# Kernel optimization log

Measured on AMD Instinct MI355X. Metric: run time of the kernel, lower is better.

Reference implementation:

```python
import jax, jax.numpy as jnp
import numpy as np

N_NODES = 50000


def gcn_conv(x, W, b, src, dst):
    # PyG GCNConv: lin (no bias) -> add self-loops -> symmetric deg norm ->
    # scatter-add messages to target nodes -> add bias.
    n = x.shape[0]
    xw = x @ W  # [N, H]
    loops = jnp.arange(n, dtype=src.dtype)
    s = jnp.concatenate([src, loops])
    d = jnp.concatenate([dst, loops])
    deg = jax.ops.segment_sum(jnp.ones(d.shape[0], dtype=x.dtype), d, num_segments=n)
    dinv = deg ** -0.5  # deg >= 1 due to self-loops
    norm = dinv[s] * dinv[d]  # [E+N]
    msg = xw[s] * norm[:, None]  # gather + scale, [E+N, H]
    out = jax.ops.segment_sum(msg, d, num_segments=n)  # scatter-add
    return out + b


def setup_inputs() -> dict:
    key = jax.random.key(0)
    ks = jax.random.split(key, 8)
    in_feats, hidden, out_feats, p = 64, 64, 32, 4
    x = jax.random.normal(ks[0], (N_NODES, in_feats), dtype=jnp.float32)
    edge_index = jax.random.randint(ks[1], (2, 800000), 0, N_NODES, dtype=jnp.int64)
    s1 = (1.0 / in_feats) ** 0.5
    s2 = (1.0 / hidden) ** 0.5
    W1 = jax.random.uniform(ks[2], (in_feats, hidden), jnp.float32, -s1, s1)
    b1 = jnp.zeros((hidden,), jnp.float32)
    W2 = jax.random.uniform(ks[3], (hidden, hidden), jnp.float32, -s2, s2)
    b2 = jnp.zeros((hidden,), jnp.float32)
    Wr = jax.random.uniform(ks[4], (hidden, out_feats * p), jnp.float32, -s2, s2)
    br = jax.random.uniform(ks[5], (out_feats * p,), jnp.float32, -s2, s2)
    return {"x": x, "edge_index": edge_index, "W1": W1, "b1": b1,
            "W2": W2, "b2": b2, "Wr": Wr, "br": br}


def reference(x, edge_index, W1, b1, W2, b2, Wr, br):
    src, dst = edge_index[0], edge_index[1]
    h = jax.nn.relu(gcn_conv(x, W1, b1, src, dst))
    h = jax.nn.relu(gcn_conv(h, W2, b2, src, dst))
    g = jnp.mean(h, axis=0, keepdims=True)  # [1, hidden]
    out = (g @ Wr + br).reshape(32, 4)  # (out_feats, p)
    return out
```

## Files before the change

### kernel.cpp

```cpp
#include <hip/hip_runtime.h>
#include <math.h>


#define CH 16384
#define MAXNB 1024

__global__ __launch_bounds__(256) void k_bucket_hist(const int* __restrict__ dst,
                                                     int* __restrict__ histmat,
                                                     int E, int NB) {
    __shared__ int ih[MAXNB];
    int t = threadIdx.x;
    for (int k = t; k < NB; k += 256) ih[k] = 0;
    __syncthreads();
    int base = blockIdx.x * CH;
    for (int i = 0; i < CH; i += 256) {
        int e = base + i + t;
        if (e < E) atomicAdd(&ih[dst[e] >> 6], 1);
    }
    __syncthreads();
    for (int k = t; k < NB; k += 256) histmat[(size_t)blockIdx.x * NB + k] = ih[k];
}

__global__ __launch_bounds__(256) void k_colscan(int* __restrict__ histmat,
                                                 int* __restrict__ tot,
                                                 int NB, int nch) {
    int k = blockIdx.x * 256 + threadIdx.x;
    if (k >= NB) return;
    int run = 0;
    for (int b = 0; b < nch; b++) {
        int v = histmat[(size_t)b * NB + k];
        histmat[(size_t)b * NB + k] = run;
        run += v;
    }
    tot[k] = run;
}

__global__ __launch_bounds__(256) void k_scanb(const int* __restrict__ tot,
                                               int* __restrict__ bstart,
                                               int* __restrict__ offsets,
                                               int NB, int E, int n) {
    __shared__ int sc[256];
    __shared__ int carry;
    int t = threadIdx.x;
    if (t == 0) carry = 0;
    __syncthreads();
    int nchunk = (NB + 255) / 256;
    for (int c = 0; c < nchunk; c++) {
        int idx = c * 256 + t;
        int v = (idx < NB) ? tot[idx] : 0;
        sc[t] = v;
        __syncthreads();
        for (int off = 1; off < 256; off <<= 1) {
            int x = (t >= off) ? sc[t - off] : 0;
            __syncthreads();
            sc[t] += x;
            __syncthreads();
        }
        if (idx < NB) bstart[idx] = sc[t] - v + carry;
        __syncthreads();
        if (t == 0) carry += sc[255];
        __syncthreads();
    }
    if (t == 0) { bstart[NB] = E; offsets[n] = E; }
}

__global__ __launch_bounds__(256) void k_bucket_scatter(const int* __restrict__ src,
                                                        const int* __restrict__ dst,
                                                        const int* __restrict__ histmat,
                                                        const int* __restrict__ bstart,
                                                        int* __restrict__ staged,
                                                        int E, int NB) {
    __shared__ int cur[MAXNB];
    int t = threadIdx.x;
    for (int k = t; k < NB; k += 256)
        cur[k] = bstart[k] + histmat[(size_t)blockIdx.x * NB + k];
    __syncthreads();
    int base = blockIdx.x * CH;
    for (int i = 0; i < CH; i += 256) {
        int e = base + i + t;
        if (e < E) {
            int d = dst[e];
            int pos = atomicAdd(&cur[d >> 6], 1);
            staged[pos] = (src[e] << 6) | (d & 63);
        }
    }
}

__global__ __launch_bounds__(256) void k_local_sort(const int* __restrict__ staged,
                                                    const int* __restrict__ bstart,
                                                    int* __restrict__ csr_src,
                                                    int* __restrict__ offsets,
                                                    float* __restrict__ dinv, int n) {
    __shared__ int cnt[64];
    __shared__ int pos[64];
    __shared__ int cur[64];
    int t = threadIdx.x;
    if (t < 64) cnt[t] = 0;
    __syncthreads();
    int k = blockIdx.x;
    int beg = bstart[k], end = bstart[k + 1];
    for (int e = beg + t; e < end; e += 256) atomicAdd(&cnt[staged[e] & 63], 1);
    __syncthreads();
    if (t == 0) {
        int run = 0;
        for (int i = 0; i < 64; i++) { pos[i] = run; run += cnt[i]; }
    }
    __syncthreads();
    if (t < 64) {
        cur[t] = pos[t];
        int node = k * 64 + t;
        if (node < n) {
            offsets[node] = beg + pos[t];
            dinv[node] = 1.0f / sqrtf((float)(cnt[t] + 1));
        }
    }
    __syncthreads();
    for (int e = beg + t; e < end; e += 256) {
        int pk = staged[e];
        int p = atomicAdd(&cur[pk & 63], 1);
        csr_src[beg + p] = pk >> 6;
    }
}

__global__ __launch_bounds__(256) void k_gemm_scale(const float* __restrict__ X,
                                                    const float* __restrict__ W,
                                                    const float* __restrict__ dinv,
                                                    float* __restrict__ Y, int n) {
    __shared__ float Ws[64 * 64];
    __shared__ float xs[16][64];
    int t = threadIdx.x, w = t >> 6, f = t & 63;
    const float4* W4 = (const float4*)W;
    float4* Ws4 = (float4*)Ws;
#pragma unroll
    for (int j = 0; j < 4; j++) Ws4[t + 256 * j] = W4[t + 256 * j];
    int r0 = blockIdx.x * 16;
#pragma unroll
    for (int i = 0; i < 4; i++) {
        int r = r0 + w * 4 + i;
        xs[w * 4 + i][f] = (r < n) ? X[(size_t)r * 64 + f] : 0.f;
    }
    __syncthreads();
    float acc[4] = {0.f, 0.f, 0.f, 0.f};
#pragma unroll 8
    for (int k = 0; k < 64; k++) {
        float wv = Ws[k * 64 + f];
#pragma unroll
        for (int i = 0; i < 4; i++) acc[i] += xs[w * 4 + i][k] * wv;
    }
#pragma unroll
    for (int i = 0; i < 4; i++) {
        int r = r0 + w * 4 + i;
        if (r < n) Y[(size_t)r * 64 + f] = dinv[r] * acc[i];
    }
}

template <bool POOL>
__global__ __launch_bounds__(256) void k_aggregate(const float* __restrict__ Y,
                                                   const float* __restrict__ dinv,
                                                   const float* __restrict__ bias,
                                                   const int* __restrict__ offsets,
                                                   const int* __restrict__ csr_src,
                                                   float* __restrict__ H,
                                                   float* __restrict__ pbuf, int n) {
    __shared__ float sm[256];
    int t = threadIdx.x, w = t >> 6, f = t & 63;
    int node = blockIdx.x * 4 + w;
    bool valid = node < n;
    float hval = 0.f;
    if (valid) {
        int beg = offsets[node], end = offsets[node + 1];
        float acc = Y[(size_t)node * 64 + f];
        for (int j = beg; j < end; j += 8) {
#pragma unroll
            for (int u = 0; u < 8; u++) {
                int jj = j + u;
                bool c = jj < end;
                int jc = c ? jj : beg;
                int s = csr_src[jc];
                float a = Y[(size_t)s * 64 + f];
                acc += c ? a : 0.f;
            }
        }
        hval = fmaxf(dinv[node] * acc + bias[f], 0.f);
        if (!POOL) H[(size_t)node * 64 + f] = hval;
    }
    if (POOL) {
        sm[t] = valid ? hval : 0.f;
        __syncthreads();
        if (w == 0) pbuf[(size_t)blockIdx.x * 64 + f] =
            sm[f] + sm[64 + f] + sm[128 + f] + sm[192 + f];
    }
}

__global__ void k_mean_final(const float* __restrict__ pbuf, float* __restrict__ g,
                             int nrows) {
    __shared__ float part[256];
    int t = threadIdx.x, w = t >> 6, f = t & 63;
    float local = 0.f;
    for (int r = blockIdx.x * 4 + w; r < nrows; r += gridDim.x * 4)
        local += pbuf[(size_t)r * 64 + f];
    part[t] = local;
    __syncthreads();
    if (w == 0) {
        float tot = part[f] + part[64 + f] + part[128 + f] + part[192 + f];
        atomicAdd(&g[f], tot);
    }
}

__global__ void k_readout(const float* __restrict__ g, const float* __restrict__ Wr,
                          const float* __restrict__ br, float* __restrict__ out,
                          float invn) {
    __shared__ float gl[64];
    int t = threadIdx.x;
    if (t < 64) gl[t] = g[t] * invn;
    __syncthreads();
    float acc = br[t];
#pragma unroll
    for (int k = 0; k < 64; k++) acc += gl[k] * Wr[k * 128 + t];
    out[t] = acc;
}

extern "C" void kernel_launch(void* const* d_in, const int* in_sizes, int n_in,
                              void* d_out, int out_size, void* d_ws, size_t ws_size,
                              hipStream_t stream) {
    const float* x  = (const float*)d_in[0];
    const int*   ei = (const int*)d_in[1];
    const float* W1 = (const float*)d_in[2];
    const float* b1 = (const float*)d_in[3];
    const float* W2 = (const float*)d_in[4];
    const float* b2 = (const float*)d_in[5];
    const float* Wr = (const float*)d_in[6];
    const float* br = (const float*)d_in[7];
    float* out = (float*)d_out;

    int n = in_sizes[0] / 64;
    int E = in_sizes[1] / 2;
    const int* src = ei;
    const int* dst = ei + E;

    int NB  = (n + 63) / 64;
    int nch = (E + CH - 1) / CH;

    char* p = (char*)d_ws;
    float* y = (float*)p;      p += (size_t)n * 64 * sizeof(float);
    float* h = (float*)p;      p += (size_t)n * 64 * sizeof(float);
    float* dinv = (float*)p;   p += (size_t)n * sizeof(float);
    float* g = (float*)p;      p += 64 * sizeof(float);
    int* staged = (int*)p;     p += (size_t)E * sizeof(int);
    int* csr_src = (int*)p;    p += (size_t)E * sizeof(int);
    int* offsets = (int*)p;    p += (size_t)(n + 1) * sizeof(int);
    int* histmat = (int*)p;    p += (size_t)nch * NB * sizeof(int);
    int* tot = (int*)p;        p += (size_t)NB * sizeof(int);
    int* bstart = (int*)p;     p += (size_t)(NB + 1) * sizeof(int);

    int gb = (n + 3) / 4;

    hipMemsetAsync(g, 0, 64 * sizeof(float), stream);
    k_bucket_hist<<<nch, 256, 0, stream>>>(dst, histmat, E, NB);
    k_colscan<<<(NB + 255) / 256, 256, 0, stream>>>(histmat, tot, NB, nch);
    k_scanb<<<1, 256, 0, stream>>>(tot, bstart, offsets, NB, E, n);
    k_bucket_scatter<<<nch, 256, 0, stream>>>(src, dst, histmat, bstart, staged, E, NB);
    k_local_sort<<<NB, 256, 0, stream>>>(staged, bstart, csr_src, offsets, dinv, n);

    k_gemm_scale<<<(n + 15) / 16, 256, 0, stream>>>(x, W1, dinv, y, n);
    k_aggregate<false><<<gb, 256, 0, stream>>>(y, dinv, b1, offsets, csr_src, h, nullptr, n);
    k_gemm_scale<<<(n + 15) / 16, 256, 0, stream>>>(h, W2, dinv, y, n);
    float* pbuf = h;
    k_aggregate<true><<<gb, 256, 0, stream>>>(y, dinv, b2, offsets, csr_src, nullptr, pbuf, n);

    k_mean_final<<<64, 256, 0, stream>>>(pbuf, g, gb);
    k_readout<<<1, 128, 0, stream>>>(g, Wr, br, out, 1.0f / (float)n);
}
```

Before: 269.1 us.

## Vectorize aggregation with float4 edge-parallel lanes and shrink histogram chunks

The aggregation kernel now assigns 16 lanes per node row with float4 loads, and splits each node's edge list across four lane groups, combining them with cross-lane shuffles. Each wavefront therefore keeps more independent gathers in flight, and each neighbour index is loaded once per group instead of once per feature lane. The histogram chunk size is reduced to raise block count, and the column scan is unrolled by 8 so its loads batch ahead of the stores. In exchange, the column scan has more chunks to walk and more partial histograms to write.

```diff
diff --git a/kernel.cpp b/kernel.cpp
--- a/kernel.cpp
+++ b/kernel.cpp
@@ -2,7 +2,7 @@
 #include <math.h>
 
 
-#define CH 16384
+#define CH 4096
 #define MAXNB 1024
 
 __global__ __launch_bounds__(256) void k_bucket_hist(const int* __restrict__ dst,
@@ -27,10 +27,22 @@
     int k = blockIdx.x * 256 + threadIdx.x;
     if (k >= NB) return;
     int run = 0;
-    for (int b = 0; b < nch; b++) {
-        int v = histmat[(size_t)b * NB + k];
+    int b = 0;
+    for (; b + 8 <= nch; b += 8) {
+        int v[8];
+#pragma unroll
+        for (int u = 0; u < 8; u++) v[u] = histmat[(size_t)(b + u) * NB + k];
+#pragma unroll
+        for (int u = 0; u < 8; u++) {
+            int x = v[u];
+            histmat[(size_t)(b + u) * NB + k] = run;
+            run += x;
+        }
+    }
+    for (; b < nch; b++) {
+        int x = histmat[(size_t)b * NB + k];
         histmat[(size_t)b * NB + k] = run;
-        run += v;
+        run += x;
     }
     tot[k] = run;
 }
@@ -162,33 +174,57 @@
                                                    const int* __restrict__ csr_src,
                                                    float* __restrict__ H,
                                                    float* __restrict__ pbuf, int n) {
-    __shared__ float sm[256];
-    int t = threadIdx.x, w = t >> 6, f = t & 63;
+    __shared__ float4 sm4[4][16];
+    const float4* Y4 = (const float4*)Y;
+    int t = threadIdx.x, w = t >> 6, l = t & 63;
+    int q = l >> 4, c = l & 15;
     int node = blockIdx.x * 4 + w;
     bool valid = node < n;
-    float hval = 0.f;
+    float4 hval = make_float4(0.f, 0.f, 0.f, 0.f);
     if (valid) {
+        float4 acc = make_float4(0.f, 0.f, 0.f, 0.f);
+        if (q == 0) acc = Y4[(size_t)node * 16 + c];
         int beg = offsets[node], end = offsets[node + 1];
-        float acc = Y[(size_t)node * 64 + f];
-        for (int j = beg; j < end; j += 8) {
-#pragma unroll
-            for (int u = 0; u < 8; u++) {
-                int jj = j + u;
-                bool c = jj < end;
-                int jc = c ? jj : beg;
-                int s = csr_src[jc];
-                float a = Y[(size_t)s * 64 + f];
-                acc += c ? a : 0.f;
+        for (int j = beg + q; j < end; j += 16) {
+#pragma unroll
+            for (int u = 0; u < 4; u++) {
+                int jj = j + 4 * u;
+                bool ok = jj < end;
+                float4 v = make_float4(0.f, 0.f, 0.f, 0.f);
+                if (ok) {
+                    int s = csr_src[jj];
+                    v = Y4[(size_t)s * 16 + c];
+                }
+                acc.x += v.x; acc.y += v.y; acc.z += v.z; acc.w += v.w;
             }
         }
-        hval = fmaxf(dinv[node] * acc + bias[f], 0.f);
-        if (!POOL) H[(size_t)node * 64 + f] = hval;
+#pragma unroll
+        for (int m = 16; m <= 32; m <<= 1) {
+            acc.x += __shfl_xor(acc.x, m);
+            acc.y += __shfl_xor(acc.y, m);
+            acc.z += __shfl_xor(acc.z, m);
+            acc.w += __shfl_xor(acc.w, m);
+        }
+        float dv = dinv[node];
+        float4 b4 = ((const float4*)bias)[c];
+        hval.x = fmaxf(dv * acc.x + b4.x, 0.f);
+        hval.y = fmaxf(dv * acc.y + b4.y, 0.f);
+        hval.z = fmaxf(dv * acc.z + b4.z, 0.f);
+        hval.w = fmaxf(dv * acc.w + b4.w, 0.f);
+        if (!POOL && q == 0) ((float4*)H)[(size_t)node * 16 + c] = hval;
     }
     if (POOL) {
-        sm[t] = valid ? hval : 0.f;
+        if (q == 0) sm4[w][c] = valid ? hval : make_float4(0.f, 0.f, 0.f, 0.f);
         __syncthreads();
-        if (w == 0) pbuf[(size_t)blockIdx.x * 64 + f] =
-            sm[f] + sm[64 + f] + sm[128 + f] + sm[192 + f];
+        if (t < 16) {
+            float4 a = sm4[0][t], b = sm4[1][t], d = sm4[2][t], e = sm4[3][t];
+            float4 s;
+            s.x = (a.x + b.x) + (d.x + e.x);
+            s.y = (a.y + b.y) + (d.y + e.y);
+            s.z = (a.z + b.z) + (d.z + e.z);
+            s.w = (a.w + b.w) + (d.w + e.w);
+            ((float4*)pbuf)[(size_t)blockIdx.x * 16 + t] = s;
+        }
     }
 }
 
```

Measured after the change: 231.6 us. 1.16x faster.
